# Kernel tuning notes

Hardware: AMD Instinct MI355X
Metric: run time of the kernel (lower is better)

## Reference

```python
import jax, jax.numpy as jnp
import numpy as np

N, E = 50000, 400000
IN_DIM = OUT_DIM = 128
T, R, H = 4, 8, 8
DK = OUT_DIM // H


def setup_inputs() -> dict:
    key = jax.random.key(0)
    ks = jax.random.split(key, 20)
    xav = lambda k, i, o: jax.random.uniform(k, (T, i, o), jnp.float32, -1.0, 1.0) * np.sqrt(6.0 / (i + o))
    return {
        "node_inp": jax.random.normal(ks[0], (N, IN_DIM), jnp.float32),
        "node_type": jax.random.randint(ks[1], (N,), 0, T),
        "edge_index": jax.random.randint(ks[2], (2, E), 0, N),
        "edge_type": jax.random.randint(ks[3], (E,), 0, R),
        "edge_sign": jax.random.randint(ks[4], (E,), 0, 3) - 1,  # values in {-1,0,1}
        "Wq": xav(ks[5], IN_DIM, OUT_DIM), "bq": jnp.zeros((T, OUT_DIM)),
        "Wk": xav(ks[6], IN_DIM, OUT_DIM), "bk": jnp.zeros((T, OUT_DIM)),
        "Wv": xav(ks[7], IN_DIM, OUT_DIM), "bv": jnp.zeros((T, OUT_DIM)),
        "rel_q": jax.random.normal(ks[8], (R, H, DK), jnp.float32),
        "rel_k": jax.random.normal(ks[9], (R, H, DK), jnp.float32),
        "rel_v": jax.random.normal(ks[10], (R, H, DK), jnp.float32),
        "sign_k_neutral": jnp.ones((H, DK), jnp.float32),
        "sign_v_neutral": jnp.ones((H, DK), jnp.float32),
        "rel_bias": jnp.zeros((R, H), jnp.float32),
        "skip": jnp.ones((T,), jnp.float32),
        "ln_gamma": jnp.ones((T, OUT_DIM), jnp.float32),
        "ln_beta": jnp.zeros((T, OUT_DIM), jnp.float32),
    }


def reference(node_inp, node_type, edge_index, edge_type, edge_sign,
              Wq, bq, Wk, bk, Wv, bv, rel_q, rel_k, rel_v,
              sign_k_neutral, sign_v_neutral, rel_bias, skip, ln_gamma, ln_beta):
    n = node_inp.shape[0]
    src, dst = edge_index[0], edge_index[1]
    rows = jnp.arange(n)
    # per-node-type linear projections: compute for all types, select by node_type
    proj = lambda W, b: (jnp.einsum('ni,tio->tno', node_inp, W) + b[:, None, :])[node_type, rows]
    Q = proj(Wq, bq).reshape(n, H, DK)
    K = proj(Wk, bk).reshape(n, H, DK)
    V = proj(Wv, bv).reshape(n, H, DK)
    # sign tables: [neg(-1), pos(+1), neutral]
    ones = jnp.ones((H, DK), node_inp.dtype)
    sign_k_all = jnp.stack([-ones, ones, sign_k_neutral], 0)
    sign_v_all = jnp.stack([-ones, ones, sign_v_neutral], 0)
    s_idx = jnp.where(edge_sign == -1, 0, jnp.where(edge_sign == 1, 1, 2))
    q_eff = Q[dst] * rel_q[edge_type]                      # [E,H,DK]
    k_eff = K[src] * rel_k[edge_type] * sign_k_all[s_idx]
    v_eff = V[src] * rel_v[edge_type] * sign_v_all[s_idx]
    scores = (q_eff * k_eff).sum(-1) / np.sqrt(DK) + rel_bias[edge_type]  # [E,H]
    # segment softmax over dst groups
    smax = jax.ops.segment_max(scores, dst, num_segments=n)
    ex = jnp.exp(scores - smax[dst])
    ssum = jax.ops.segment_sum(ex, dst, num_segments=n)
    attn = ex / (ssum[dst] + 1e-16)
    msg = (v_eff * attn[..., None]).reshape(-1, OUT_DIM)
    out = jnp.zeros((n, OUT_DIM), node_inp.dtype).at[dst].add(msg)
    # per-type gated skip + layernorm
    alpha = jax.nn.sigmoid(skip)[node_type][:, None]
    pre = alpha * out + (1.0 - alpha) * node_inp
    mu = pre.mean(-1, keepdims=True)
    var = ((pre - mu) ** 2).mean(-1, keepdims=True)
    normed = (pre - mu) / jnp.sqrt(var + 1e-5)
    return normed * ln_gamma[node_type] + ln_beta[node_type]
```

## Files before the change

### kernel.cpp

```cpp
#include <hip/hip_runtime.h>
#include <hip/hip_bf16.h>


#define D 128
#define NT 4
#define NR 8
#define NH 8
#define SCAN_BS 256

typedef unsigned short ushort_t;
typedef unsigned int uint_t;

static __device__ __forceinline__ ushort_t f2bf(float f) {
    uint_t u = __float_as_uint(f);
    return (ushort_t)((u + 0x7FFFu + ((u >> 16) & 1u)) >> 16);
}
static __device__ __forceinline__ float bf2f(ushort_t h) {
    return __uint_as_float(((uint_t)h) << 16);
}

__global__ void k_hist_n(const int* __restrict__ nt, int N, int* __restrict__ tcnt) {
    __shared__ int lcnt[NT];
    int tid = threadIdx.x;
    if (tid < NT) lcnt[tid] = 0;
    __syncthreads();
    int g = blockIdx.x * 256 + tid;
    if (g < N) atomicAdd(&lcnt[nt[g]], 1);
    __syncthreads();
    if (tid < NT && lcnt[tid]) atomicAdd(&tcnt[tid], lcnt[tid]);
}

__global__ void k_hist_e(const int* __restrict__ ei, int E, int* __restrict__ deg) {
    int g = blockIdx.x * 256 + threadIdx.x;
    if (g < E) atomicAdd(&deg[ei[E + g]], 1);
}

__global__ __launch_bounds__(SCAN_BS) void k_scan1(const int* __restrict__ deg, int N,
                                                   int* __restrict__ bsum) {
    __shared__ int lds[SCAN_BS];
    int ti = threadIdx.x;
    int i = blockIdx.x * SCAN_BS + ti;
    lds[ti] = (i < N) ? deg[i] : 0;
    __syncthreads();
    for (int off = SCAN_BS >> 1; off > 0; off >>= 1) {
        if (ti < off) lds[ti] += lds[ti + off];
        __syncthreads();
    }
    if (ti == 0) bsum[blockIdx.x] = lds[0];
}

__global__ __launch_bounds__(SCAN_BS) void k_scan2(const int* __restrict__ bsum, int NB,
                                                   const int* __restrict__ tcnt,
                                                   int* __restrict__ bbase,
                                                   int* __restrict__ toff,
                                                   int* __restrict__ row_ptr, int N, int E) {
    __shared__ int lds[SCAN_BS];
    int ti = threadIdx.x;
    int v = (ti < NB) ? bsum[ti] : 0;
    lds[ti] = v;
    __syncthreads();
    for (int off = 1; off < SCAN_BS; off <<= 1) {
        int t = (ti >= off) ? lds[ti - off] : 0;
        __syncthreads();
        lds[ti] += t;
        __syncthreads();
    }
    if (ti < NB) bbase[ti] = lds[ti] - v;
    if (ti == 0) {
        int a = 0;
        for (int t = 0; t < NT; t++) { toff[t] = a; a += tcnt[t]; }
        toff[NT] = a;
        row_ptr[N] = E;
    }
}

__global__ __launch_bounds__(SCAN_BS) void k_scan3(const int* __restrict__ deg, int N,
                                                   const int* __restrict__ bbase,
                                                   int* __restrict__ row_ptr,
                                                   int* __restrict__ ecur) {
    __shared__ int lds[SCAN_BS];
    int ti = threadIdx.x;
    int i = blockIdx.x * SCAN_BS + ti;
    int v = (i < N) ? deg[i] : 0;
    lds[ti] = v;
    __syncthreads();
    for (int off = 1; off < SCAN_BS; off <<= 1) {
        int t = (ti >= off) ? lds[ti - off] : 0;
        __syncthreads();
        lds[ti] += t;
        __syncthreads();
    }
    if (i < N) {
        int ex = bbase[blockIdx.x] + lds[ti] - v;
        row_ptr[i] = ex;
        ecur[i] = ex;
    }
}

__global__ void k_scat_n(const int* __restrict__ nt, int N, int* __restrict__ tcur,
                         const int* __restrict__ toff, int* __restrict__ sorted) {
    __shared__ int lcnt[NT];
    __shared__ int lbase[NT];
    int tid = threadIdx.x;
    if (tid < NT) lcnt[tid] = 0;
    __syncthreads();
    int g = blockIdx.x * 256 + tid;
    int t = -1, myrank = 0;
    if (g < N) {
        t = nt[g];
        myrank = atomicAdd(&lcnt[t], 1);
    }
    __syncthreads();
    if (tid < NT) lbase[tid] = lcnt[tid] ? atomicAdd(&tcur[tid], lcnt[tid]) : 0;
    __syncthreads();
    if (t >= 0) sorted[toff[t] + lbase[t] + myrank] = g;
}

__global__ void k_scat_e(const int* __restrict__ ei, const int* __restrict__ et,
                         const int* __restrict__ es, int E,
                         int* __restrict__ ecur, int* __restrict__ csr_rec) {
    int g = blockIdx.x * 256 + threadIdx.x;
    if (g < E) {
        int src = ei[g];
        int d = ei[E + g];
        int r = et[g];
        int sg = es[g];
        int p = atomicAdd(&ecur[d], 1);
        csr_rec[p] = src | (r << 17) | ((sg + 1) << 20);
    }
}

__global__ __launch_bounds__(512, 4) void k_proj(
    const float* __restrict__ x, const int* __restrict__ sorted,
    const int* __restrict__ toff,
    const float* __restrict__ Wq, const float* __restrict__ bq,
    const float* __restrict__ Wk, const float* __restrict__ bk,
    const float* __restrict__ Wv, const float* __restrict__ bv,
    float* __restrict__ Q, ushort_t* __restrict__ Kb, ushort_t* __restrict__ Vb) {
    __shared__ float xs[128 * 129];
    __shared__ int sid[128];
    int tid = threadIdx.x;
    int b = blockIdx.x;
    int t = -1, p0 = 0;
    int cum = 0;
    for (int tt = 0; tt < NT; tt++) {
        int cnt_t = toff[tt + 1] - toff[tt];
        int nb = (cnt_t + 127) >> 7;
        if (t < 0 && b < cum + nb) { t = tt; p0 = toff[tt] + (b - cum) * 128; }
        cum += nb;
    }
    if (t < 0) return;
    int cnt = min(128, toff[t + 1] - p0);

    if (tid < 128) sid[tid] = (tid < cnt) ? sorted[p0 + tid] : -1;
    __syncthreads();
    for (int j = 0; j < 8; j++) {
        int idx = j * 512 + tid;
        int row = idx >> 5, c4 = (idx & 31) * 4;
        int node = sid[row];
        if (node >= 0) {
            float4 v = *(const float4*)(x + (size_t)node * D + c4);
            float* p = &xs[row * 129 + c4];
            p[0] = v.x; p[1] = v.y; p[2] = v.z; p[3] = v.w;
        }
    }
    __syncthreads();

    int og = tid & 15, ng = tid >> 4;
    int o0 = og * 8;
    int m = blockIdx.y;
    const float* Wm = (m == 0) ? Wq : (m == 1) ? Wk : Wv;
    const float* bm = (m == 0) ? bq : (m == 1) ? bk : bv;
    Wm += (size_t)t * D * D;
    bm += t * D;

    float acc[4][8];
    float bias[8];
#pragma unroll
    for (int c = 0; c < 8; c++) bias[c] = bm[o0 + c];
#pragma unroll
    for (int r = 0; r < 4; r++)
#pragma unroll
        for (int c = 0; c < 8; c++) acc[r][c] = bias[c];

#pragma unroll 4
    for (int k = 0; k < D; k++) {
        float4 w0 = *(const float4*)(Wm + k * D + o0);
        float4 w1 = *(const float4*)(Wm + k * D + o0 + 4);
        float w8[8] = {w0.x, w0.y, w0.z, w0.w, w1.x, w1.y, w1.z, w1.w};
        float xv[4];
#pragma unroll
        for (int r = 0; r < 4; r++) xv[r] = xs[(ng * 4 + r) * 129 + k];
#pragma unroll
        for (int r = 0; r < 4; r++)
#pragma unroll
            for (int c = 0; c < 8; c++) acc[r][c] += xv[r] * w8[c];
    }
#pragma unroll
    for (int r = 0; r < 4; r++) {
        int node = sid[ng * 4 + r];
        if (node < 0) continue;
        if (m == 0) {
            float4 a0 = {acc[r][0], acc[r][1], acc[r][2], acc[r][3]};
            float4 a1 = {acc[r][4], acc[r][5], acc[r][6], acc[r][7]};
            *(float4*)(Q + (size_t)node * D + o0) = a0;
            *(float4*)(Q + (size_t)node * D + o0 + 4) = a1;
        } else {
            ushort_t* Om = (m == 1) ? Kb : Vb;
            uint_t p[4];
#pragma unroll
            for (int c = 0; c < 4; c++)
                p[c] = (uint_t)f2bf(acc[r][2 * c]) | ((uint_t)f2bf(acc[r][2 * c + 1]) << 16);
            uint4 pk = {p[0], p[1], p[2], p[3]};
            *(uint4*)(Om + (size_t)node * D + o0) = pk;
        }
    }
}

__global__ __launch_bounds__(256) void k_agg(
    const int* __restrict__ row_ptr, const int* __restrict__ csr_rec,
    const int* __restrict__ nt, const float* __restrict__ x,
    const float* __restrict__ Qt, const ushort_t* __restrict__ Kb,
    const ushort_t* __restrict__ Vb, const float* __restrict__ rq,
    const float* __restrict__ rk, const float* __restrict__ rv,
    const float* __restrict__ skn, const float* __restrict__ svn,
    const float* __restrict__ rb, const float* __restrict__ skip,
    const float* __restrict__ gamma, const float* __restrict__ beta,
    float* __restrict__ out, int N) {
    __shared__ float l_rq[NR * 132];
    __shared__ float l_rk[NR * 132];
    __shared__ float l_rv[NR * 132];
    __shared__ float l_rb[NR * NH];
    int tid = threadIdx.x;
    for (int idx = tid; idx < NR * D; idx += 256) {
        int r = idx >> 7, c = idx & 127;
        l_rq[r * 132 + c] = rq[idx];
        l_rk[r * 132 + c] = rk[idx];
        l_rv[r * 132 + c] = rv[idx];
    }
    if (tid < NR * NH) l_rb[tid] = rb[tid];
    __syncthreads();

    int wid = (blockIdx.x * 256 + tid) >> 6;
    if (wid >= N) return;
    int lane = tid & 63;
    int h = lane >> 3, li = lane & 7;
    int d0 = lane * 2;
    int dst = wid;
    int rp0 = row_ptr[dst];
    int deg = row_ptr[dst + 1] - rp0;

    float4 q4[4], sk4[4];
#pragma unroll
    for (int j = 0; j < 4; j++) {
        q4[j] = *(const float4*)(Qt + (size_t)dst * D + h * 16 + 4 * j);
        sk4[j] = *(const float4*)(skn + h * 16 + 4 * j);
    }
    float2 sv2 = *(const float2*)(svn + d0);
    float2 xi = *(const float2*)(x + (size_t)dst * D + d0);
    int t = nt[dst];

    float m = -INFINITY, lsum = 0.f, acc0 = 0.f, acc1 = 0.f;

    for (int c0 = 0; c0 < deg; c0 += 8) {
        int cn = min(8, deg - c0);
        bool valid = li < cn;
        int recA = csr_rec[rp0 + c0 + (valid ? li : 0)];
        int srcA = recA & 0x1FFFF;
        int rA = (recA >> 17) & 7;
        int sgA = ((recA >> 20) & 3) - 1;
        bool neuA = (sgA == 0);
        float fsgA = (float)sgA;
        const ushort_t* kp = Kb + (size_t)srcA * D + h * 16;
        const float* rqp = &l_rq[rA * 132 + h * 16];
        const float* rkp = &l_rk[rA * 132 + h * 16];
        float dot = 0.f;
#pragma unroll
        for (int j = 0; j < 4; j++) {
            ushort4 kk = ((const ushort4*)kp)[j];
            float k0 = bf2f(kk.x), k1 = bf2f(kk.y), k2 = bf2f(kk.z), k3 = bf2f(kk.w);
            float4 a4 = *(const float4*)(rqp + 4 * j);
            float4 b4 = *(const float4*)(rkp + 4 * j);
            float f0 = neuA ? sk4[j].x : fsgA;
            float f1 = neuA ? sk4[j].y : fsgA;
            float f2 = neuA ? sk4[j].z : fsgA;
            float f3 = neuA ? sk4[j].w : fsgA;
            dot += q4[j].x * a4.x * k0 * b4.x * f0;
            dot += q4[j].y * a4.y * k1 * b4.y * f1;
            dot += q4[j].z * a4.z * k2 * b4.z * f2;
            dot += q4[j].w * a4.w * k3 * b4.w * f3;
        }
        float scA = valid ? dot * 0.25f + l_rb[rA * NH + h] : -INFINITY;
        float cm = scA;
        cm = fmaxf(cm, __shfl_xor(cm, 1));
        cm = fmaxf(cm, __shfl_xor(cm, 2));
        cm = fmaxf(cm, __shfl_xor(cm, 4));
        float nm = fmaxf(m, cm);
        float resc = __expf(m - nm);
        acc0 *= resc; acc1 *= resc; lsum *= resc;
        m = nm;
        int rec_[8];
        float w_[8];
        uint_t v2_[8];
#pragma unroll
        for (int i = 0; i < 8; i++) {
            rec_[i] = __shfl(recA, i);
            int src = rec_[i] & 0x1FFFF;
            v2_[i] = *(const uint_t*)(Vb + (size_t)src * D + d0);
            float s = __shfl(scA, (lane & 56) | i);
            w_[i] = __expf(s - m);
        }
#pragma unroll
        for (int i = 0; i < 8; i++) {
            float w = w_[i];
            lsum += w;
            int r = (rec_[i] >> 17) & 7;
            int sg = ((rec_[i] >> 20) & 3) - 1;
            float v0 = bf2f((ushort_t)(v2_[i] & 0xFFFF));
            float v1 = bf2f((ushort_t)(v2_[i] >> 16));
            float2 r2 = *(const float2*)(&l_rv[r * 132 + d0]);
            bool neu = (sg == 0);
            float f0 = neu ? sv2.x : (float)sg;
            float f1 = neu ? sv2.y : (float)sg;
            acc0 += w * v0 * r2.x * f0;
            acc1 += w * v1 * r2.y * f1;
        }
    }
    float winv = 1.f / (lsum + 1e-16f);
    float a0 = acc0 * winv, a1 = acc1 * winv;

    float alpha = 1.f / (1.f + __expf(-skip[t]));
    float p0 = alpha * a0 + (1.f - alpha) * xi.x;
    float p1 = alpha * a1 + (1.f - alpha) * xi.y;
    float rs = p0 + p1, rsq = p0 * p0 + p1 * p1;
#pragma unroll
    for (int o = 1; o < 64; o <<= 1) {
        rs += __shfl_xor(rs, o);
        rsq += __shfl_xor(rsq, o);
    }
    float mu = rs * (1.f / 128.f);
    float var = rsq * (1.f / 128.f) - mu * mu;
    float rstd = rsqrtf(var + 1e-5f);
    float2 g2 = *(const float2*)(gamma + t * D + d0);
    float2 b2 = *(const float2*)(beta + t * D + d0);
    float o0 = (p0 - mu) * rstd * g2.x + b2.x;
    float o1 = (p1 - mu) * rstd * g2.y + b2.y;
    *(float2*)(out + (size_t)dst * D + d0) = make_float2(o0, o1);
}

extern "C" void kernel_launch(void* const* d_in, const int* in_sizes, int n_in,
                              void* d_out, int out_size, void* d_ws, size_t ws_size,
                              hipStream_t stream) {
    const float* x   = (const float*)d_in[0];
    const int*  nt   = (const int*)d_in[1];
    const int*  ei   = (const int*)d_in[2];
    const int*  et   = (const int*)d_in[3];
    const int*  es   = (const int*)d_in[4];
    const float* Wq  = (const float*)d_in[5];
    const float* bq  = (const float*)d_in[6];
    const float* Wk  = (const float*)d_in[7];
    const float* bk  = (const float*)d_in[8];
    const float* Wv  = (const float*)d_in[9];
    const float* bv  = (const float*)d_in[10];
    const float* rq  = (const float*)d_in[11];
    const float* rk  = (const float*)d_in[12];
    const float* rv  = (const float*)d_in[13];
    const float* skn = (const float*)d_in[14];
    const float* svn = (const float*)d_in[15];
    const float* rb  = (const float*)d_in[16];
    const float* skp = (const float*)d_in[17];
    const float* gma = (const float*)d_in[18];
    const float* bta = (const float*)d_in[19];
    float* out = (float*)d_out;

    int N = in_sizes[0] / D;
    int E = in_sizes[2] / 2;
    int NB = (N + SCAN_BS - 1) / SCAN_BS;

    float*    Q  = (float*)d_ws;
    ushort_t* Kb = (ushort_t*)(Q + (size_t)N * D);
    ushort_t* Vb = Kb + (size_t)N * D;
    int* deg     = (int*)(Vb + (size_t)N * D);
    int* tcnt    = deg + N;
    int* tcur    = tcnt + NT;
    int* row_ptr = tcur + NT;
    int* ecur    = row_ptr + N + 1;
    int* toff    = ecur + N;
    int* sorted  = toff + 8;
    int* csr_rec = sorted + N;
    int* bsum    = csr_rec + E;
    int* bbase   = bsum + NB;

    hipMemsetAsync(deg, 0, (size_t)(N + 2 * NT) * sizeof(int), stream);

    int gbN = (N + 255) / 256;
    int gbE = (E + 255) / 256;
    k_hist_n<<<gbN, 256, 0, stream>>>(nt, N, tcnt);
    k_hist_e<<<gbE, 256, 0, stream>>>(ei, E, deg);
    k_scan1<<<NB, SCAN_BS, 0, stream>>>(deg, N, bsum);
    k_scan2<<<1, SCAN_BS, 0, stream>>>(bsum, NB, tcnt, bbase, toff, row_ptr, N, E);
    k_scan3<<<NB, SCAN_BS, 0, stream>>>(deg, N, bbase, row_ptr, ecur);
    k_scat_n<<<gbN, 256, 0, stream>>>(nt, N, tcur, toff, sorted);
    k_scat_e<<<gbE, 256, 0, stream>>>(ei, et, es, E, ecur, csr_rec);
    int nbp = (N + 127) / 128 + NT;
    k_proj<<<dim3(nbp, 3), 512, 0, stream>>>(x, sorted, toff, Wq, bq, Wk, bk,
                                             Wv, bv, Q, Kb, Vb);
    k_agg<<<(N * 64 + 255) / 256, 256, 0, stream>>>(row_ptr, csr_rec, nt, x, Q, Kb, Vb,
                                                    rq, rk, rv, skn, svn, rb, skp,
                                                    gma, bta, out, N);
}
```

Before: 340.4 us.

## Use split-bf16 MFMA for per-type projections and fuse histogram/scatter kernels

The per-type Q/K/V projection moves from scalar fp32 FMAs on LDS tiles to 16x16x32 bf16 MFMA instructions. Three products (hi*hi, hi*lo, lo*hi) keep accuracy close to fp32. New prep kernels split the weights (transposed) and the type-sorted node features into hi/lo bf16 buffers in the workspace. The node and edge histogram kernels are merged, as are the node and edge scatter kernels, to cut launches. The cost is extra prep passes that write about 25MB, and epilogue stores that are now scalar and less coalesced.

```diff
diff --git a/kernel.cpp b/kernel.cpp
--- a/kernel.cpp
+++ b/kernel.cpp
@@ -10,6 +10,8 @@
 
 typedef unsigned short ushort_t;
 typedef unsigned int uint_t;
+typedef __attribute__((ext_vector_type(8))) short short8v;
+typedef __attribute__((ext_vector_type(4))) float f32x4;
 
 static __device__ __forceinline__ ushort_t f2bf(float f) {
     uint_t u = __float_as_uint(f);
@@ -19,20 +21,17 @@
     return __uint_as_float(((uint_t)h) << 16);
 }
 
-__global__ void k_hist_n(const int* __restrict__ nt, int N, int* __restrict__ tcnt) {
+__global__ void k_hist(const int* __restrict__ nt, const int* __restrict__ ei,
+                       int N, int E, int* __restrict__ tcnt, int* __restrict__ deg) {
     __shared__ int lcnt[NT];
     int tid = threadIdx.x;
     if (tid < NT) lcnt[tid] = 0;
     __syncthreads();
     int g = blockIdx.x * 256 + tid;
     if (g < N) atomicAdd(&lcnt[nt[g]], 1);
+    if (g < E) atomicAdd(&deg[ei[E + g]], 1);
     __syncthreads();
     if (tid < NT && lcnt[tid]) atomicAdd(&tcnt[tid], lcnt[tid]);
-}
-
-__global__ void k_hist_e(const int* __restrict__ ei, int E, int* __restrict__ deg) {
-    int g = blockIdx.x * 256 + threadIdx.x;
-    if (g < E) atomicAdd(&deg[ei[E + g]], 1);
 }
 
 __global__ __launch_bounds__(SCAN_BS) void k_scan1(const int* __restrict__ deg, int N,
@@ -97,8 +96,11 @@
     }
 }
 
-__global__ void k_scat_n(const int* __restrict__ nt, int N, int* __restrict__ tcur,
-                         const int* __restrict__ toff, int* __restrict__ sorted) {
+__global__ void k_scatter(const int* __restrict__ nt, const int* __restrict__ ei,
+                          const int* __restrict__ et, const int* __restrict__ es,
+                          int N, int E, int* __restrict__ tcur,
+                          const int* __restrict__ toff, int* __restrict__ sorted,
+                          int* __restrict__ ecur, int* __restrict__ csr_rec) {
     __shared__ int lcnt[NT];
     __shared__ int lbase[NT];
     int tid = threadIdx.x;
@@ -114,12 +116,7 @@
     if (tid < NT) lbase[tid] = lcnt[tid] ? atomicAdd(&tcur[tid], lcnt[tid]) : 0;
     __syncthreads();
     if (t >= 0) sorted[toff[t] + lbase[t] + myrank] = g;
-}
-
-__global__ void k_scat_e(const int* __restrict__ ei, const int* __restrict__ et,
-                         const int* __restrict__ es, int E,
-                         int* __restrict__ ecur, int* __restrict__ csr_rec) {
-    int g = blockIdx.x * 256 + threadIdx.x;
+
     if (g < E) {
         int src = ei[g];
         int d = ei[E + g];
@@ -130,14 +127,48 @@
     }
 }
 
-__global__ __launch_bounds__(512, 4) void k_proj(
-    const float* __restrict__ x, const int* __restrict__ sorted,
-    const int* __restrict__ toff,
-    const float* __restrict__ Wq, const float* __restrict__ bq,
-    const float* __restrict__ Wk, const float* __restrict__ bk,
-    const float* __restrict__ Wv, const float* __restrict__ bv,
+__global__ void k_wprep(const float* __restrict__ Wq, const float* __restrict__ Wk,
+                        const float* __restrict__ Wv,
+                        ushort_t* __restrict__ wt_hi, ushort_t* __restrict__ wt_lo) {
+    int g = blockIdx.x * 256 + threadIdx.x;
+    if (g >= 3 * NT * D * D) return;
+    int o = g & 127;
+    int k = (g >> 7) & 127;
+    int t = (g >> 14) & 3;
+    int m = g >> 16;
+    const float* Wsel = (m == 0) ? Wq : (m == 1) ? Wk : Wv;
+    float w = Wsel[((size_t)t * D + k) * D + o];
+    ushort_t hi = f2bf(w);
+    ushort_t lo = f2bf(w - bf2f(hi));
+    size_t dst = (((size_t)(m * NT + t) * D) + o) * D + k;
+    wt_hi[dst] = hi;
+    wt_lo[dst] = lo;
+}
+
+__global__ void k_xprep(const float* __restrict__ x, const int* __restrict__ sorted,
+                        int N, ushort_t* __restrict__ xs_hi, ushort_t* __restrict__ xs_lo) {
+    int g = blockIdx.x * 256 + threadIdx.x;
+    if (g >= N * 32) return;
+    int i = g >> 5;
+    int c4 = (g & 31) * 4;
+    int node = sorted[i];
+    float4 v = *(const float4*)(x + (size_t)node * D + c4);
+    ushort4 h, l;
+    h.x = f2bf(v.x); l.x = f2bf(v.x - bf2f(h.x));
+    h.y = f2bf(v.y); l.y = f2bf(v.y - bf2f(h.y));
+    h.z = f2bf(v.z); l.z = f2bf(v.z - bf2f(h.z));
+    h.w = f2bf(v.w); l.w = f2bf(v.w - bf2f(h.w));
+    *(ushort4*)(xs_hi + (size_t)i * D + c4) = h;
+    *(ushort4*)(xs_lo + (size_t)i * D + c4) = l;
+}
+
+__global__ __launch_bounds__(512) void k_projm(
+    const ushort_t* __restrict__ xs_hi, const ushort_t* __restrict__ xs_lo,
+    const ushort_t* __restrict__ wt_hi, const ushort_t* __restrict__ wt_lo,
+    const int* __restrict__ sorted, const int* __restrict__ toff,
+    const float* __restrict__ bq, const float* __restrict__ bk,
+    const float* __restrict__ bv,
     float* __restrict__ Q, ushort_t* __restrict__ Kb, ushort_t* __restrict__ Vb) {
-    __shared__ float xs[128 * 129];
     __shared__ int sid[128];
     int tid = threadIdx.x;
     int b = blockIdx.x;
@@ -150,69 +181,76 @@
         cum += nb;
     }
     if (t < 0) return;
-    int cnt = min(128, toff[t + 1] - p0);
-
-    if (tid < 128) sid[tid] = (tid < cnt) ? sorted[p0 + tid] : -1;
-    __syncthreads();
-    for (int j = 0; j < 8; j++) {
-        int idx = j * 512 + tid;
-        int row = idx >> 5, c4 = (idx & 31) * 4;
-        int node = sid[row];
-        if (node >= 0) {
-            float4 v = *(const float4*)(x + (size_t)node * D + c4);
-            float* p = &xs[row * 129 + c4];
-            p[0] = v.x; p[1] = v.y; p[2] = v.z; p[3] = v.w;
-        }
-    }
-    __syncthreads();
-
-    int og = tid & 15, ng = tid >> 4;
-    int o0 = og * 8;
+    int tend = toff[t + 1];
+    if (tid < 128) sid[tid] = (p0 + tid < tend) ? sorted[p0 + tid] : -1;
+    __syncthreads();
+
+    int w = tid >> 6, lane = tid & 63;
+    int wr = w >> 2, wc = w & 3;
+    int l15 = lane & 15, kq = lane >> 4;
     int m = blockIdx.y;
-    const float* Wm = (m == 0) ? Wq : (m == 1) ? Wk : Wv;
+
+    const ushort_t* wth = wt_hi + ((size_t)(m * NT + t) * D) * D;
+    const ushort_t* wtl = wt_lo + ((size_t)(m * NT + t) * D) * D;
+
+    f32x4 acc[4][2];
+#pragma unroll
+    for (int fa = 0; fa < 4; fa++)
+#pragma unroll
+        for (int fb = 0; fb < 2; fb++) acc[fa][fb] = 0.f;
+
+#pragma unroll
+    for (int k0 = 0; k0 < D; k0 += 32) {
+        int kk = k0 + kq * 8;
+        short8v ah[4], al[4];
+#pragma unroll
+        for (int fa = 0; fa < 4; fa++) {
+            size_t row = (size_t)(p0 + wr * 64 + fa * 16 + l15);
+            ah[fa] = *(const short8v*)(xs_hi + row * D + kk);
+            al[fa] = *(const short8v*)(xs_lo + row * D + kk);
+        }
+        short8v bh[2], bl[2];
+#pragma unroll
+        for (int fb = 0; fb < 2; fb++) {
+            size_t col = (size_t)(wc * 32 + fb * 16 + l15);
+            bh[fb] = *(const short8v*)(wth + col * D + kk);
+            bl[fb] = *(const short8v*)(wtl + col * D + kk);
+        }
+#pragma unroll
+        for (int fa = 0; fa < 4; fa++)
+#pragma unroll
+            for (int fb = 0; fb < 2; fb++) {
+                acc[fa][fb] = __builtin_amdgcn_mfma_f32_16x16x32_bf16(
+                    al[fa], bh[fb], acc[fa][fb], 0, 0, 0);
+                acc[fa][fb] = __builtin_amdgcn_mfma_f32_16x16x32_bf16(
+                    ah[fa], bl[fb], acc[fa][fb], 0, 0, 0);
+                acc[fa][fb] = __builtin_amdgcn_mfma_f32_16x16x32_bf16(
+                    ah[fa], bh[fb], acc[fa][fb], 0, 0, 0);
+            }
+    }
+
     const float* bm = (m == 0) ? bq : (m == 1) ? bk : bv;
-    Wm += (size_t)t * D * D;
     bm += t * D;
-
-    float acc[4][8];
-    float bias[8];
-#pragma unroll
-    for (int c = 0; c < 8; c++) bias[c] = bm[o0 + c];
-#pragma unroll
-    for (int r = 0; r < 4; r++)
-#pragma unroll
-        for (int c = 0; c < 8; c++) acc[r][c] = bias[c];
-
-#pragma unroll 4
-    for (int k = 0; k < D; k++) {
-        float4 w0 = *(const float4*)(Wm + k * D + o0);
-        float4 w1 = *(const float4*)(Wm + k * D + o0 + 4);
-        float w8[8] = {w0.x, w0.y, w0.z, w0.w, w1.x, w1.y, w1.z, w1.w};
-        float xv[4];
-#pragma unroll
-        for (int r = 0; r < 4; r++) xv[r] = xs[(ng * 4 + r) * 129 + k];
-#pragma unroll
-        for (int r = 0; r < 4; r++)
-#pragma unroll
-            for (int c = 0; c < 8; c++) acc[r][c] += xv[r] * w8[c];
-    }
-#pragma unroll
-    for (int r = 0; r < 4; r++) {
-        int node = sid[ng * 4 + r];
-        if (node < 0) continue;
-        if (m == 0) {
-            float4 a0 = {acc[r][0], acc[r][1], acc[r][2], acc[r][3]};
-            float4 a1 = {acc[r][4], acc[r][5], acc[r][6], acc[r][7]};
-            *(float4*)(Q + (size_t)node * D + o0) = a0;
-            *(float4*)(Q + (size_t)node * D + o0 + 4) = a1;
-        } else {
-            ushort_t* Om = (m == 1) ? Kb : Vb;
-            uint_t p[4];
-#pragma unroll
-            for (int c = 0; c < 4; c++)
-                p[c] = (uint_t)f2bf(acc[r][2 * c]) | ((uint_t)f2bf(acc[r][2 * c + 1]) << 16);
-            uint4 pk = {p[0], p[1], p[2], p[3]};
-            *(uint4*)(Om + (size_t)node * D + o0) = pk;
+    float bias0 = bm[wc * 32 + l15];
+    float bias1 = bm[wc * 32 + 16 + l15];
+#pragma unroll
+    for (int fa = 0; fa < 4; fa++) {
+#pragma unroll
+        for (int reg = 0; reg < 4; reg++) {
+            int local = wr * 64 + fa * 16 + kq * 4 + reg;
+            int node = sid[local];
+            if (node < 0) continue;
+            float v0 = acc[fa][0][reg] + bias0;
+            float v1 = acc[fa][1][reg] + bias1;
+            int col0 = wc * 32 + l15;
+            if (m == 0) {
+                Q[(size_t)node * D + col0] = v0;
+                Q[(size_t)node * D + col0 + 16] = v1;
+            } else {
+                ushort_t* Om = (m == 1) ? Kb : Vb;
+                Om[(size_t)node * D + col0] = f2bf(v0);
+                Om[(size_t)node * D + col0 + 16] = f2bf(v1);
+            }
         }
     }
 }
@@ -377,10 +415,14 @@
     int E = in_sizes[2] / 2;
     int NB = (N + SCAN_BS - 1) / SCAN_BS;
 
-    float*    Q  = (float*)d_ws;
-    ushort_t* Kb = (ushort_t*)(Q + (size_t)N * D);
-    ushort_t* Vb = Kb + (size_t)N * D;
-    int* deg     = (int*)(Vb + (size_t)N * D);
+    float*    Q     = (float*)d_ws;
+    ushort_t* Kb    = (ushort_t*)(Q + (size_t)N * D);
+    ushort_t* Vb    = Kb + (size_t)N * D;
+    ushort_t* xs_hi = Vb + (size_t)N * D;
+    ushort_t* xs_lo = xs_hi + (size_t)N * D;
+    ushort_t* wt_hi = xs_lo + (size_t)N * D;
+    ushort_t* wt_lo = wt_hi + (size_t)3 * NT * D * D;
+    int* deg     = (int*)(wt_lo + (size_t)3 * NT * D * D);
     int* tcnt    = deg + N;
     int* tcur    = tcnt + NT;
     int* row_ptr = tcur + NT;
@@ -393,18 +435,18 @@
 
     hipMemsetAsync(deg, 0, (size_t)(N + 2 * NT) * sizeof(int), stream);
 
-    int gbN = (N + 255) / 256;
-    int gbE = (E + 255) / 256;
-    k_hist_n<<<gbN, 256, 0, stream>>>(nt, N, tcnt);
-    k_hist_e<<<gbE, 256, 0, stream>>>(ei, E, deg);
+    int gbNE = (max(N, E) + 255) / 256;
+    k_wprep<<<(3 * NT * D * D + 255) / 256, 256, 0, stream>>>(Wq, Wk, Wv, wt_hi, wt_lo);
+    k_hist<<<gbNE, 256, 0, stream>>>(nt, ei, N, E, tcnt, deg);
     k_scan1<<<NB, SCAN_BS, 0, stream>>>(deg, N, bsum);
     k_scan2<<<1, SCAN_BS, 0, stream>>>(bsum, NB, tcnt, bbase, toff, row_ptr, N, E);
     k_scan3<<<NB, SCAN_BS, 0, stream>>>(deg, N, bbase, row_ptr, ecur);
-    k_scat_n<<<gbN, 256, 0, stream>>>(nt, N, tcur, toff, sorted);
-    k_scat_e<<<gbE, 256, 0, stream>>>(ei, et, es, E, ecur, csr_rec);
+    k_scatter<<<gbNE, 256, 0, stream>>>(nt, ei, et, es, N, E, tcur, toff, sorted,
+                                        ecur, csr_rec);
+    k_xprep<<<(N * 32 + 255) / 256, 256, 0, stream>>>(x, sorted, N, xs_hi, xs_lo);
     int nbp = (N + 127) / 128 + NT;
-    k_proj<<<dim3(nbp, 3), 512, 0, stream>>>(x, sorted, toff, Wq, bq, Wk, bk,
-                                             Wv, bv, Q, Kb, Vb);
+    k_projm<<<dim3(nbp, 3), 512, 0, stream>>>(xs_hi, xs_lo, wt_hi, wt_lo, sorted,
+                                              toff, bq, bk, bv, Q, Kb, Vb);
     k_agg<<<(N * 64 + 255) / 256, 256, 0, stream>>>(row_ptr, csr_rec, nt, x, Q, Kb, Vb,
                                                     rq, rk, rv, skn, svn, rb, skp,
                                                     gma, bta, out, N);
```

Result: faster. 330.1 us (-3.0%).
